# Optimization experiments

Measured on AMD Instinct MI355X. Metric: run time of the kernel, lower is better.

## Reference

```python
import jax, jax.numpy as jnp
import numpy as np

C, K, N = 128, 27, 4096   # channels, kernel offsets (3^3), parent points
M = 8 * N                  # child points (FCG: up to 8 children per parent)


def sp_conv(f, nbr, W):
    # sparse submanifold conv: gather K neighbors then per-offset GEMM
    # f: [P, C], nbr: [P, K], W: [K, C, C] -> [P, C]
    return jnp.einsum('pkc,kcd->pd', f[nbr], W)


def resnet(f, nbr, Wa, Wb):
    h = jax.nn.relu(sp_conv(f, nbr, Wa))
    return jax.nn.relu(sp_conv(h, nbr, Wb) + f)


def setup_inputs():
    key = jax.random.key(0)
    ks = jax.random.split(key, 30)
    conv = lambda k: jax.random.normal(k, (K, C, C), dtype=jnp.float32) * 0.02
    return {
        'x_O': jax.random.randint(ks[0], (N,), 0, 256, dtype=jnp.int32),
        'gt_O': jax.random.randint(ks[1], (M, 1), 0, 256, dtype=jnp.int32),
        'nbr_par': jax.random.randint(ks[2], (N, K), 0, N, dtype=jnp.int32),
        'nbr_child': jax.random.randint(ks[3], (M, K), 0, M, dtype=jnp.int32),
        'child_oct': jnp.tile(jnp.arange(8, dtype=jnp.int32), N),
        'prior_emb': jax.random.normal(ks[4], (256, C), dtype=jnp.float32),
        'pW0': conv(ks[5]), 'pW1a': conv(ks[6]), 'pW1b': conv(ks[7]),
        'pW2a': conv(ks[8]), 'pW2b': conv(ks[9]),
        'oct_emb': jax.random.normal(ks[10], (8, C), dtype=jnp.float32) * 0.1,
        'tW0': conv(ks[11]), 'tW1a': conv(ks[12]), 'tW1b': conv(ks[13]),
        'tW2a': conv(ks[14]), 'tW2b': conv(ks[15]),
        's1_emb': jax.random.normal(ks[16], (16, C), dtype=jnp.float32) * 0.1,
        'h0W1': jax.random.normal(ks[17], (C, C), dtype=jnp.float32) * 0.09,
        'h0b1': jnp.zeros((C,), dtype=jnp.float32),
        'h0W2': jax.random.normal(ks[18], (C, 16), dtype=jnp.float32) * 0.09,
        'h0b2': jnp.zeros((16,), dtype=jnp.float32),
        'h1W1': jax.random.normal(ks[19], (C, C), dtype=jnp.float32) * 0.09,
        'h1b1': jnp.zeros((C,), dtype=jnp.float32),
        'h1W2': jax.random.normal(ks[20], (C, 16), dtype=jnp.float32) * 0.09,
        'h1b2': jnp.zeros((16,), dtype=jnp.float32),
    }


def reference(x_O, gt_O, nbr_par, nbr_child, child_oct,
              prior_emb, pW0, pW1a, pW1b, pW2a, pW2b,
              oct_emb, tW0, tW1a, tW1b, tW2a, tW2b, s1_emb,
              h0W1, h0b1, h0W2, h0b2, h1W1, h1b1, h1W2, h1b2):
    # prior branch: occupancy byte embedding + sparse ResNet stack
    f = prior_emb[x_O]                                   # [N, C]
    f = jax.nn.relu(sp_conv(f, nbr_par, pW0))
    f = resnet(f, nbr_par, pW1a, pW1b)
    f = resnet(f, nbr_par, pW2a, pW2b)
    # FCG: broadcast parent feature to its 8 children; TargetEmbedding adds octant embedding
    g = jnp.repeat(f, 8, axis=0) + oct_emb[child_oct]    # [M, C]
    g = jax.nn.relu(sp_conv(g, nbr_child, tW0))
    g = resnet(g, nbr_child, tW1a, tW1b)
    g = resnet(g, nbr_child, tW2a, tW2b)
    # two-stage 4-bit occupancy prediction + gather-based entropy
    gt_s0 = jnp.remainder(gt_O, 16)                      # [M, 1]
    gt_s1 = gt_O // 16
    p0 = jax.nn.softmax(jax.nn.relu(g @ h0W1 + h0b1) @ h0W2 + h0b2, axis=-1)
    g1 = g + s1_emb[gt_s0[:, 0]]
    p1 = jax.nn.softmax(jax.nn.relu(g1 @ h1W1 + h1b1) @ h1W2 + h1b2, axis=-1)
    b0 = jnp.take_along_axis(p0, gt_s0, axis=1)
    b1 = jnp.take_along_axis(p1, gt_s1, axis=1)
    bits = (jnp.sum(jnp.clip(-jnp.log2(b0 + 1e-10), 0.0, 50.0))
            + jnp.sum(jnp.clip(-jnp.log2(b1 + 1e-10), 0.0, 50.0)))
    return bits / jnp.float32(N)
```

## Files before the change

kernel.cpp:

```cpp
#include <hip/hip_runtime.h>

typedef unsigned int u32;
typedef unsigned short u16;
typedef unsigned char u8;
typedef short bf16x8 __attribute__((ext_vector_type(8)));
typedef float f32x4 __attribute__((ext_vector_type(4)));
typedef unsigned short u16x4 __attribute__((ext_vector_type(4)));
typedef long lx2 __attribute__((ext_vector_type(2)));

#define KOFF 27

__device__ __forceinline__ float bf2f(u16 u) {
    u32 x = ((u32)u) << 16;
    return __builtin_bit_cast(float, x);
}
__device__ __forceinline__ u16 f2bf(float f) {
    u32 u = __builtin_bit_cast(u32, f);
    u32 r = (u + 0x7FFFu + ((u >> 16) & 1u)) >> 16;
    return (u16)r;
}
__device__ __forceinline__ u8 f2fp8(float f) {
    u32 u = __builtin_bit_cast(u32, f);
    u32 sign = (u >> 24) & 0x80u;
    float a = fabsf(f);
    if (a >= 448.f) return (u8)(sign | 0x7Eu);
    if (a < 0.015625f) {
        int q = (int)rintf(a * 512.f);
        return (u8)(sign | (u32)q);
    }
    u32 m = u & 0x7FFFFFFFu;
    m += 0x7FFFFu + ((m >> 20) & 1u);
    u32 e8 = (m >> 23) - 120u;
    if (e8 >= 16u) return (u8)(sign | 0x7Eu);
    return (u8)(sign | (e8 << 3) | ((m >> 20) & 7u));
}
__device__ __forceinline__ float fp82f(u8 v) {
    u32 s = ((u32)(v & 0x80)) << 24;
    u32 em = v & 0x7Fu;
    float mag;
    if (em < 8)
        mag = (float)em * 0.001953125f;
    else
        mag = __builtin_bit_cast(float,
                                 (((em >> 3) + 120u) << 23) | ((em & 7u) << 20));
    return __builtin_bit_cast(float, __builtin_bit_cast(u32, mag) | s);
}
__device__ __forceinline__ void async16(void* lds, const void* g) {
    __builtin_amdgcn_global_load_lds(
        (const __attribute__((address_space(1))) u32*)g,
        (__attribute__((address_space(3))) u32*)lds, 16, 0, 0);
}

struct PrepArgs {
    const float* ws[12];
    u16* wd[12];
    u8* wd3[5];
    const float* h0W2;
    const float* h1W2;
    u16* wt2h;
    const float* s1emb;
    const float* h1W1f;
    float* E1;
};
__global__ __launch_bounds__(256) void prep_mega(PrepArgs a) {
    __shared__ float t[128][65];
    const int bid = blockIdx.x;
    if (bid < 270) {
        const int w = bid / 54, r = bid % 54;
        const int k = r >> 1, cg = r & 1;
        const float* s = a.ws[w] + k * 16384 + cg * 64;
        for (int i = threadIdx.x; i < 8192; i += 256) {
            int c = i >> 6, dl = i & 63;
            t[c][dl] = s[c * 128 + dl];
        }
        __syncthreads();
        u16* ob = a.wd[w] + k * 16384;
        for (int sl = threadIdx.x; sl < 1024; sl += 256) {
            int lane = sl & 63, kk2 = (sl >> 6) & 1, n = (sl >> 7) & 3,
                kslc = (sl >> 9) & 1;
            int S = (((kslc * 2 + cg) * 4 + n) * 2 + kk2) * 64 + lane;
            int dl = n * 16 + (lane & 15);
            int c0 = kslc * 64 + kk2 * 32 + (lane >> 4) * 8;
            u16x4 v0, v1;
#pragma unroll
            for (int j = 0; j < 4; ++j) v0[j] = f2bf(t[c0 + j][dl]);
#pragma unroll
            for (int j = 0; j < 4; ++j) v1[j] = f2bf(t[c0 + 4 + j][dl]);
            *(u16x4*)(ob + S * 8) = v0;
            *(u16x4*)(ob + S * 8 + 4) = v1;
        }
    } else if (bid < 540) {
        const int idx = bid - 270;
        const int w5 = idx / 54, r = idx % 54;
        const int k = r >> 1, cg = r & 1;
        const float* s = a.ws[5 + w5] + k * 16384 + cg * 64;
        for (int i = threadIdx.x; i < 8192; i += 256) {
            int c = i >> 6, dl = i & 63;
            t[c][dl] = s[c * 128 + dl];
        }
        __syncthreads();
        u8* ob = a.wd3[w5] + k * 16384;
        for (int sl = threadIdx.x; sl < 8192; sl += 256) {
            int j = sl & 7, lane = (sl >> 3) & 63, kk2 = (sl >> 9) & 1,
                n = (sl >> 10) & 3, kslc = (sl >> 12) & 1;
            int c = kslc * 64 + kk2 * 32 + (lane >> 4) * 8 + j;
            int dl = n * 16 + (lane & 15);
            int byte = (kslc * 2 + cg) * 4096 + n * 1024 + lane * 16 + kk2 * 8 + j;
            ob[byte] = f2fp8(t[c][dl]);
        }
    } else if (bid < 544) {
        int r = bid - 540;
        int w = 10 + (r >> 1), half = r & 1;
        const float* s = a.ws[w] + half * 64;
        for (int i = threadIdx.x; i < 8192; i += 256) {
            int c = i >> 6, dl = i & 63;
            t[c][dl] = s[c * 128 + dl];
        }
        __syncthreads();
        u16* db = a.wd[w];
        for (int i = threadIdx.x; i < 8192; i += 256) {
            int dl = i >> 7, c = i & 127;
            int d = half * 64 + dl;
            db[d * 128 + (c ^ ((d & 7) << 3))] = f2bf(t[c][dl]);
        }
    } else if (bid < 546) {
        int h = bid - 544;
        const float* src = h ? a.h1W2 : a.h0W2;
        u16* dst = a.wt2h + h * 2048;
        for (int i = threadIdx.x; i < 2048; i += 256) {
            int j = i >> 7, d = i & 127;
            dst[j * 128 + (d ^ ((j & 7) << 3))] = f2bf(src[d * 16 + j]);
        }
    } else {
        int b = bid - 546;
        int r = b * 2 + (threadIdx.x >> 7);
        int c = threadIdx.x & 127;
        float acc = 0.f;
        for (int kx = 0; kx < 128; ++kx)
            acc = fmaf(a.s1emb[r * 128 + kx], a.h1W1f[kx * 128 + c], acc);
        a.E1[r * 128 + c] = acc;
    }
}

__global__ __launch_bounds__(256) void embed_k(const int* __restrict__ xO,
                                               const float* __restrict__ emb,
                                               u16* __restrict__ out) {
    int idx = blockIdx.x * 256 + threadIdx.x;
    int c = idx & 127, n = idx >> 7;
    out[idx] = f2bf(emb[xO[n] * 128 + c]);
}

__global__ __launch_bounds__(256) void expand8(const u16* __restrict__ f,
                                               const int* __restrict__ oct,
                                               const float* __restrict__ oemb,
                                               u8* __restrict__ g) {
    int idx = blockIdx.x * 256 + threadIdx.x;
    int c = idx & 127, m = idx >> 7;
    g[idx] = f2fp8(bf2f(f[(m >> 3) * 128 + c]) + oemb[oct[m] * 128 + c]);
}

#define LOADB(dst, vb, imm)                                      \
    asm volatile("global_load_dwordx4 %0, %1, %2 offset:" #imm   \
                 : "=&v"(dst)                                    \
                 : "v"(vb), "s"(wk)                              \
                 : "memory")

template <bool PARTIAL>
__global__ __launch_bounds__(256, 2) void conv7(
    const u16* __restrict__ fin, const int* __restrict__ nbr,
    const u16* __restrict__ wt, const u16* __restrict__ res,
    u16* __restrict__ fout, float* __restrict__ pout, int npts) {
    constexpr int BM = 64;
    __shared__ __align__(16) u16 Asb[2][4][4096];
    __shared__ int nbrS[BM * KOFF];
    const int tid = threadIdx.x;
    const int wid = tid >> 6;
    const int lane = tid & 63;
    const int p0 = blockIdx.x * BM;
    const int g = PARTIAL ? blockIdx.y : 0;
    const int k0 = PARTIAL ? (g * KOFF) >> 3 : 0;
    const int k1 = PARTIAL ? ((g + 1) * KOFF) >> 3 : KOFF;

    for (int i = tid; i < BM * KOFF; i += 256)
        nbrS[i] = nbr[(p0 + i / KOFF) * KOFF + (i % KOFF)];
    __syncthreads();

    f32x4 acc[2][4];
#pragma unroll
    for (int m = 0; m < 2; ++m)
#pragma unroll
        for (int n = 0; n < 4; ++n) acc[m][n] = f32x4{0.f, 0.f, 0.f, 0.f};

    const int rg0 = (wid >> 1) * 32;
    const int cg = wid & 1;
    const int lrow = lane & 15;
    const int lkb = (lane >> 4) * 16;
    const int b0a = cg * 8192 + lane * 16;
    const int b0b = b0a + 4096;
    const int b1a = b0a + 16384;
    const int b1b = b1a + 4096;

    auto stageA = [&](int k, int buf) {
        char* db = (char*)&Asb[buf][wid][0];
#pragma unroll
        for (int i = 0; i < 8; ++i) {
            int rl = i * 4 + (lane >> 4);
            int cbs = ((lane & 15) * 16) ^ ((rl & 7) << 4);
            int rgl = nbrS[(rg0 + rl) * KOFF + k];
            async16(db + i * 1024, (const char*)fin + (size_t)rgl * 256 + cbs);
        }
    };
    auto loadB = [&](int k, bf16x8 (&B)[16]) {
        const u16* wk = wt + k * 16384;
        LOADB(B[0], b0a, 0);
        LOADB(B[1], b0a, 1024);
        LOADB(B[2], b1a, 0);
        LOADB(B[3], b1a, 1024);
        LOADB(B[4], b0a, 2048);
        LOADB(B[5], b0a, 3072);
        LOADB(B[6], b1a, 2048);
        LOADB(B[7], b1a, 3072);
        LOADB(B[8], b0b, 0);
        LOADB(B[9], b0b, 1024);
        LOADB(B[10], b1b, 0);
        LOADB(B[11], b1b, 1024);
        LOADB(B[12], b0b, 2048);
        LOADB(B[13], b0b, 3072);
        LOADB(B[14], b1b, 2048);
        LOADB(B[15], b1b, 3072);
    };

    bf16x8 Ba[16], Bb[16];
    stageA(k0, 0);
    loadB(k0, Ba);

    auto body = [&](bf16x8 (&Bc)[16], bf16x8 (&Bn)[16], int k) {
        const int ab = (k - k0) & 1;
        if (k + 1 < k1) {
            stageA(k + 1, ab ^ 1);
            loadB(k + 1, Bn);
            asm volatile("s_waitcnt vmcnt(24)" ::: "memory");
        } else {
            asm volatile("s_waitcnt vmcnt(0)" ::: "memory");
        }
        __builtin_amdgcn_sched_barrier(0);
        const char* AsW = (const char*)&Asb[ab][wid][0];
        __builtin_amdgcn_s_setprio(1);
#pragma unroll
        for (int kk = 0; kk < 4; ++kk) {
            bf16x8 av[2];
#pragma unroll
            for (int m = 0; m < 2; ++m) {
                int row = m * 16 + lrow;
                int cb = (kk * 64 + lkb) ^ ((row & 7) << 4);
                av[m] = *(const bf16x8*)(AsW + row * 256 + cb);
            }
#pragma unroll
            for (int m = 0; m < 2; ++m)
#pragma unroll
                for (int n = 0; n < 4; ++n)
                    acc[m][n] = __builtin_amdgcn_mfma_f32_16x16x32_bf16(
                        av[m], Bc[n * 4 + kk], acc[m][n], 0, 0, 0);
        }
        __builtin_amdgcn_s_setprio(0);
    };

    int k = k0;
    while (true) {
        body(Ba, Bb, k);
        if (++k >= k1) break;
        body(Bb, Ba, k);
        if (++k >= k1) break;
    }

    if constexpr (PARTIAL) {
        float* pg = pout + (size_t)g * npts * 128;
#pragma unroll
        for (int m = 0; m < 2; ++m) {
            int prow = p0 + rg0 + m * 16 + (lane >> 4) * 4;
#pragma unroll
            for (int n = 0; n < 4; ++n) {
                int dcol = cg * 64 + n * 16 + lrow;
#pragma unroll
                for (int q = 0; q < 4; ++q)
                    pg[(prow + q) * 128 + dcol] = acc[m][n][q];
            }
        }
    } else {
#pragma unroll
        for (int m = 0; m < 2; ++m) {
            int prow = p0 + rg0 + m * 16 + (lane >> 4) * 4;
#pragma unroll
            for (int n = 0; n < 4; ++n) {
                int dcol = cg * 64 + n * 16 + lrow;
#pragma unroll
                for (int q = 0; q < 4; ++q) {
                    float v = acc[m][n][q];
                    int p = prow + q;
                    if (res) v += bf2f(res[p * 128 + dcol]);
                    v = v > 0.f ? v : 0.f;
                    fout[p * 128 + dcol] = f2bf(v);
                }
            }
        }
    }
}

template <bool LASTBF16>
__global__ __launch_bounds__(256, 4) void conv9(
    const u8* __restrict__ fin, const int* __restrict__ nbr,
    const u8* __restrict__ wt, const u8* __restrict__ res,
    void* __restrict__ fout_) {
    constexpr int BM = 32;
    __shared__ __align__(16) u8 Asb[2][BM * 128];
    __shared__ float red[4096];
    __shared__ int nbrS[BM * KOFF];
    const int tid = threadIdx.x;
    const int wid = tid >> 6;
    const int lane = tid & 63;
    const int p0 = blockIdx.x * BM;

    for (int i = tid; i < BM * KOFF; i += 256)
        nbrS[i] = nbr[(p0 + i / KOFF) * KOFF + (i % KOFF)];
    __syncthreads();

    f32x4 acc[2][4];
#pragma unroll
    for (int m = 0; m < 2; ++m)
#pragma unroll
        for (int n = 0; n < 4; ++n) acc[m][n] = f32x4{0.f, 0.f, 0.f, 0.f};

    const int kslc = wid >> 1;
    const int CB = (wid & 1) * 64;
    const int lrow = lane & 15;
    const int vb = (kslc * 2 + (wid & 1)) * 4096 + lane * 16;

    auto stageA = [&](int k, int buf) {
        int rl = wid * 8 + (lane >> 3);
        int boff = (lane & 7) * 16;
        int rg = nbrS[rl * KOFF + k];
        async16((char*)&Asb[buf][0] + wid * 1024,
                (const char*)fin + (size_t)rg * 128 + (boff ^ ((rl & 7) << 4)));
    };
    auto loadB = [&](int k, lx2 (&B)[4]) {
        const u8* wk = wt + k * 16384;
        LOADB(B[0], vb, 0);
        LOADB(B[1], vb, 1024);
        LOADB(B[2], vb, 2048);
        LOADB(B[3], vb, 3072);
    };

    lx2 Ba4[4], Bb4[4];
    stageA(0, 0);
    loadB(0, Ba4);

    auto body = [&](lx2 (&Bc)[4], lx2 (&Bn)[4], int k) {
        const int ab = k & 1;
        __builtin_amdgcn_s_barrier();
        if (k + 1 < KOFF) {
            loadB(k + 1, Bn);
            stageA(k + 1, ab ^ 1);
            asm volatile("s_waitcnt vmcnt(5)" ::: "memory");
        } else {
            asm volatile("s_waitcnt vmcnt(0)" ::: "memory");
        }
        __builtin_amdgcn_s_barrier();
        __builtin_amdgcn_sched_barrier(0);
        __builtin_amdgcn_s_setprio(1);
#pragma unroll
        for (int kk2 = 0; kk2 < 2; ++kk2) {
            long av[2];
#pragma unroll
            for (int m = 0; m < 2; ++m) {
                int row = m * 16 + lrow;
                int off = (kslc * 64 + kk2 * 32 + (lane >> 4) * 8) ^
                          ((row & 7) << 4);
                av[m] = *(const long*)((const char*)&Asb[ab][0] + row * 128 + off);
            }
#pragma unroll
            for (int m = 0; m < 2; ++m)
#pragma unroll
                for (int n = 0; n < 4; ++n)
                    acc[m][n] = __builtin_amdgcn_mfma_f32_16x16x32_fp8_fp8(
                        av[m], Bc[n][kk2], acc[m][n], 0, 0, 0);
        }
        __builtin_amdgcn_s_setprio(0);
    };

    int k = 0;
    while (true) {
        body(Ba4, Bb4, k);
        if (++k >= KOFF) break;
        body(Bb4, Ba4, k);
        if (++k >= KOFF) break;
    }

    __syncthreads();
    if (kslc == 1) {
        const int base = (wid - 2) * 2048;
#pragma unroll
        for (int m = 0; m < 2; ++m)
#pragma unroll
            for (int n = 0; n < 4; ++n)
#pragma unroll
                for (int q = 0; q < 4; ++q)
                    red[base + (((m * 4 + n) * 4 + q) * 64) + lane] =
                        acc[m][n][q];
    }
    __syncthreads();
    if (kslc == 0) {
        const int base = wid * 2048;
#pragma unroll
        for (int m = 0; m < 2; ++m)
#pragma unroll
            for (int n = 0; n < 4; ++n)
#pragma unroll
                for (int q = 0; q < 4; ++q)
                    acc[m][n][q] +=
                        red[base + (((m * 4 + n) * 4 + q) * 64) + lane];
#pragma unroll
        for (int m = 0; m < 2; ++m) {
            int prow = p0 + m * 16 + (lane >> 4) * 4;
#pragma unroll
            for (int n = 0; n < 4; ++n) {
                int dcol = CB + n * 16 + lrow;
#pragma unroll
                for (int q = 0; q < 4; ++q) {
                    float v = acc[m][n][q];
                    int p = prow + q;
                    if (res) v += fp82f(res[p * 128 + dcol]);
                    v = v > 0.f ? v : 0.f;
                    if constexpr (LASTBF16)
                        ((u16*)fout_)[p * 128 + dcol] = f2bf(v);
                    else
                        ((u8*)fout_)[p * 128 + dcol] = f2fp8(v);
                }
            }
        }
    }
}

__global__ __launch_bounds__(256) void combine_k(const float* __restrict__ P,
                                                 const u16* __restrict__ res,
                                                 u16* __restrict__ fout,
                                                 int nelem) {
    int base = (blockIdx.x * 256 + threadIdx.x) * 4;
    f32x4 s = *(const f32x4*)(P + base);
#pragma unroll
    for (int gg = 1; gg < 8; ++gg)
        s += *(const f32x4*)(P + (size_t)gg * nelem + base);
    u16x4 o;
    if (res) {
        u16x4 rv = *(const u16x4*)(res + base);
#pragma unroll
        for (int j = 0; j < 4; ++j) s[j] += bf2f(rv[j]);
    }
#pragma unroll
    for (int j = 0; j < 4; ++j) {
        float v = s[j] > 0.f ? s[j] : 0.f;
        o[j] = f2bf(v);
    }
    *(u16x4*)(fout + base) = o;
}

__global__ __launch_bounds__(512, 1) void fused_heads(
    const u16* __restrict__ G, const int* __restrict__ gtO,
    const u16* __restrict__ wt2, const u16* __restrict__ wt2h,
    const float* __restrict__ b1a, const float* __restrict__ b1b,
    const float* __restrict__ E1, const float* __restrict__ b2a,
    const float* __restrict__ b2b, float* __restrict__ partial) {
    __shared__ __align__(16) u16 AB[49152];
    __shared__ __align__(16) u16 W2ts[4096];
    __shared__ float E1s[2048];
    __shared__ float b2s[32];
    __shared__ int gts[256];
    __shared__ float bitsS[256];
    u16* Asb = AB;
    u16* Bsb = AB + 16384;
    char* Hb = (char*)AB;
    const int tid = threadIdx.x, wid = tid >> 6, lane = tid & 63;
    const int lrow = lane & 15, lkb = (lane >> 4) * 16;
    const int p0 = blockIdx.x * 128;

#pragma unroll
    for (int i = 0; i < 4; ++i) {
        int o = i * 8192 + tid * 16;
        int r = o >> 8;
        int cbs = (o & 255) ^ ((r & 7) << 4);
        async16((char*)Asb + i * 8192 + wid * 1024,
                (const char*)G + (size_t)(p0 + r) * 256 + cbs);
    }
#pragma unroll
    for (int i = 0; i < 8; ++i)
        async16((char*)Bsb + i * 8192 + wid * 1024,
                (const char*)wt2 + i * 8192 + tid * 16);
    async16((char*)W2ts + wid * 1024, (const char*)wt2h + tid * 16);
    for (int i = tid; i < 2048; i += 512) E1s[i] = E1[i];
    if (tid < 16) b2s[tid] = b2a[tid];
    else if (tid < 32) b2s[tid] = b2b[tid - 16];
    if (tid < 128) {
        int g = gtO[p0 + tid];
        gts[tid] = g & 15;
        gts[128 + tid] = g >> 4;
    }
    __syncthreads();

    const int RB = (wid >> 1) * 32, CB = (wid & 1) * 128;
    f32x4 acc[2][8];
#pragma unroll
    for (int m = 0; m < 2; ++m)
#pragma unroll
        for (int n = 0; n < 8; ++n) acc[m][n] = f32x4{0.f, 0.f, 0.f, 0.f};
    __builtin_amdgcn_s_setprio(1);
#pragma unroll
    for (int kk = 0; kk < 4; ++kk) {
        bf16x8 av[2], bv[8];
#pragma unroll
        for (int m = 0; m < 2; ++m) {
            int row = RB + m * 16 + lrow;
            int cb = (kk * 64 + lkb) ^ ((row & 7) << 4);
            av[m] = *(const bf16x8*)((const char*)Asb + row * 256 + cb);
        }
#pragma unroll
        for (int n = 0; n < 8; ++n) {
            int drow = CB + n * 16 + lrow;
            int cb = (kk * 64 + lkb) ^ ((drow & 7) << 4);
            bv[n] = *(const bf16x8*)((const char*)Bsb + drow * 256 + cb);
        }
#pragma unroll
        for (int m = 0; m < 2; ++m)
#pragma unroll
            for (int n = 0; n < 8; ++n)
                acc[m][n] = __builtin_amdgcn_mfma_f32_16x16x32_bf16(
                    av[m], bv[n], acc[m][n], 0, 0, 0);
    }
    __builtin_amdgcn_s_setprio(0);
    __syncthreads();

    const float* b1p = CB ? b1b : b1a;
    float b1v[8];
#pragma unroll
    for (int n = 0; n < 8; ++n) b1v[n] = b1p[n * 16 + lrow];
#pragma unroll
    for (int m = 0; m < 2; ++m) {
#pragma unroll
        for (int q = 0; q < 4; ++q) {
            int p = RB + m * 16 + (lane >> 4) * 4 + q;
#pragma unroll
            for (int n = 0; n < 8; ++n) {
                float v = acc[m][n][q] + b1v[n];
                if (CB) v += E1s[gts[p] * 128 + n * 16 + lrow];
                v = v > 0.f ? v : 0.f;
                int colb = (CB + n * 16 + lrow) * 2;
                *(u16*)(Hb + p * 512 + (colb ^ ((p & 7) << 4))) = f2bf(v);
            }
        }
    }
    __syncthreads();

    const int RB2 = wid * 16;
    f32x4 acc2[2];
    acc2[0] = f32x4{0.f, 0.f, 0.f, 0.f};
    acc2[1] = f32x4{0.f, 0.f, 0.f, 0.f};
#pragma unroll
    for (int kk = 0; kk < 4; ++kk) {
        int row = RB2 + lrow;
        int cb = (kk * 64 + lkb) ^ ((row & 7) << 4);
        int cbw = (kk * 64 + lkb) ^ ((lrow & 7) << 4);
#pragma unroll
        for (int h = 0; h < 2; ++h) {
            bf16x8 a2 = *(const bf16x8*)(Hb + row * 512 + h * 256 + cb);
            bf16x8 b2v = *(const bf16x8*)((const char*)W2ts + h * 4096 +
                                          lrow * 256 + cbw);
            acc2[h] = __builtin_amdgcn_mfma_f32_16x16x32_bf16(a2, b2v, acc2[h],
                                                              0, 0, 0);
        }
    }
    const int jj = lrow;
#pragma unroll
    for (int h = 0; h < 2; ++h) {
#pragma unroll
        for (int q = 0; q < 4; ++q) {
            int pt = RB2 + (lane >> 4) * 4 + q;
            float v = acc2[h][q] + b2s[h * 16 + jj];
            float mx = v;
#pragma unroll
            for (int o = 1; o < 16; o <<= 1) mx = fmaxf(mx, __shfl_xor(mx, o, 16));
            float e = expf(v - mx);
            float s = e;
#pragma unroll
            for (int o = 1; o < 16; o <<= 1) s += __shfl_xor(s, o, 16);
            float bits = -log2f(e / s + 1e-10f);
            bits = fminf(fmaxf(bits, 0.f), 50.f);
            if (jj == gts[h * 128 + pt]) bitsS[h * 128 + pt] = bits;
        }
    }
    __syncthreads();
    if (tid < 64) {
        float s = bitsS[tid] + bitsS[tid + 64] + bitsS[tid + 128] + bitsS[tid + 192];
#pragma unroll
        for (int o = 32; o > 0; o >>= 1) s += __shfl_down(s, o, 64);
        if (tid == 0) partial[blockIdx.x] = s;
    }
}

__global__ __launch_bounds__(256) void finalize_k(const float* __restrict__ partial,
                                                  float* __restrict__ out, int n) {
    float s = 0.f;
    for (int i = threadIdx.x; i < n; i += 256) s += partial[i];
#pragma unroll
    for (int o = 32; o > 0; o >>= 1) s += __shfl_down(s, o, 64);
    __shared__ float wsum[4];
    if ((threadIdx.x & 63) == 0) wsum[threadIdx.x >> 6] = s;
    __syncthreads();
    if (threadIdx.x == 0)
        out[0] = (wsum[0] + wsum[1] + wsum[2] + wsum[3]) * (1.0f / 4096.0f);
}

extern "C" void kernel_launch(void* const* d_in, const int* in_sizes, int n_in,
                              void* d_out, int out_size, void* d_ws,
                              size_t ws_size, hipStream_t stream) {
    const int N = 4096, M = 32768;
    const int* x_O = (const int*)d_in[0];
    const int* gt_O = (const int*)d_in[1];
    const int* nbr_par = (const int*)d_in[2];
    const int* nbr_ch = (const int*)d_in[3];
    const int* child_oct = (const int*)d_in[4];
    const float* prior_emb = (const float*)d_in[5];
    const float* convW[10] = {
        (const float*)d_in[6],  (const float*)d_in[7],  (const float*)d_in[8],
        (const float*)d_in[9],  (const float*)d_in[10], (const float*)d_in[12],
        (const float*)d_in[13], (const float*)d_in[14], (const float*)d_in[15],
        (const float*)d_in[16]};
    const float* oct_emb = (const float*)d_in[11];
    const float* s1_emb = (const float*)d_in[17];
    const float* h0W1 = (const float*)d_in[18];
    const float* h0b1 = (const float*)d_in[19];
    const float* h0W2 = (const float*)d_in[20];
    const float* h0b2 = (const float*)d_in[21];
    const float* h1W1 = (const float*)d_in[22];
    const float* h1b1 = (const float*)d_in[23];
    const float* h1W2 = (const float*)d_in[24];
    const float* h1b2 = (const float*)d_in[25];

    char* ws = (char*)d_ws;
    size_t off = 0;
    auto alloc = [&](size_t b) {
        void* p = ws + off;
        off += (b + 255) & ~(size_t)255;
        return p;
    };
    PrepArgs pa;
    for (int i = 0; i < 10; ++i) pa.ws[i] = convW[i];
    for (int i = 0; i < 5; ++i) pa.wd[i] = (u16*)alloc(27 * 128 * 128 * 2);
    for (int i = 5; i < 10; ++i) pa.wd[i] = nullptr;
    for (int i = 0; i < 5; ++i) pa.wd3[i] = (u8*)alloc(27 * 128 * 128);
    u16* Wt2 = (u16*)alloc(256 * 128 * 2);
    pa.ws[10] = h0W1;
    pa.ws[11] = h1W1;
    pa.wd[10] = Wt2;
    pa.wd[11] = Wt2 + 128 * 128;
    u16* wt2h = (u16*)alloc(2 * 16 * 128 * 2);
    float* E1 = (float*)alloc(16 * 128 * 4);
    pa.h0W2 = h0W2;
    pa.h1W2 = h1W2;
    pa.wt2h = wt2h;
    pa.s1emb = s1_emb;
    pa.h1W1f = h1W1;
    pa.E1 = E1;

    u16* fA = (u16*)alloc((size_t)N * 256);
    u16* fB = (u16*)alloc((size_t)N * 256);
    u16* fC = (u16*)alloc((size_t)N * 256);
    u8* g8A = (u8*)alloc((size_t)M * 128);
    u8* g8B = (u8*)alloc((size_t)M * 128);
    u8* g8C = (u8*)alloc((size_t)M * 128);
    u16* gBF = (u16*)alloc((size_t)M * 256);
    float* partial = (float*)alloc(256 * 4);
    float* pconv = (float*)g8A;

    prep_mega<<<554, 256, 0, stream>>>(pa);
    embed_k<<<N * 128 / 256, 256, 0, stream>>>(x_O, prior_emb, fA);

    const int PE = N * 128;
    conv7<true><<<dim3(64, 8), 256, 0, stream>>>(fA, nbr_par, pa.wd[0], nullptr, nullptr, pconv, N);
    combine_k<<<PE / 1024, 256, 0, stream>>>(pconv, nullptr, fB, PE);
    conv7<true><<<dim3(64, 8), 256, 0, stream>>>(fB, nbr_par, pa.wd[1], nullptr, nullptr, pconv, N);
    combine_k<<<PE / 1024, 256, 0, stream>>>(pconv, nullptr, fC, PE);
    conv7<true><<<dim3(64, 8), 256, 0, stream>>>(fC, nbr_par, pa.wd[2], nullptr, nullptr, pconv, N);
    combine_k<<<PE / 1024, 256, 0, stream>>>(pconv, fB, fA, PE);
    conv7<true><<<dim3(64, 8), 256, 0, stream>>>(fA, nbr_par, pa.wd[3], nullptr, nullptr, pconv, N);
    combine_k<<<PE / 1024, 256, 0, stream>>>(pconv, nullptr, fC, PE);
    conv7<true><<<dim3(64, 8), 256, 0, stream>>>(fC, nbr_par, pa.wd[4], nullptr, nullptr, pconv, N);
    combine_k<<<PE / 1024, 256, 0, stream>>>(pconv, fA, fB, PE);

    expand8<<<M * 128 / 256, 256, 0, stream>>>(fB, child_oct, oct_emb, g8A);

    conv9<false><<<1024, 256, 0, stream>>>(g8A, nbr_ch, pa.wd3[0], nullptr, g8B);
    conv9<false><<<1024, 256, 0, stream>>>(g8B, nbr_ch, pa.wd3[1], nullptr, g8C);
    conv9<false><<<1024, 256, 0, stream>>>(g8C, nbr_ch, pa.wd3[2], g8B, g8A);
    conv9<false><<<1024, 256, 0, stream>>>(g8A, nbr_ch, pa.wd3[3], nullptr, g8C);
    conv9<true><<<1024, 256, 0, stream>>>(g8C, nbr_ch, pa.wd3[4], g8A, gBF);

    fused_heads<<<M / 128, 512, 0, stream>>>(gBF, gt_O, Wt2, wt2h, h0b1, h1b1,
                                             E1, h0b2, h1b2, partial);
    finalize_k<<<1, 256, 0, stream>>>(partial, (float*)d_out, 256);

    (void)in_sizes; (void)n_in; (void)out_size; (void)ws_size;
}
```

Before: 301.5 us.

## Shrink child conv tile to 16 rows with two-wave K-split blocks

Replaces the 32-row, 4-wave child-conv kernel with a 16-row, 2-wave variant. Each wave covers all 128 output columns for its half of the input channels and loads twice as many weight fragments. The grid doubles to 2048 blocks, which should improve occupancy and load balance across CUs and shrink LDS use per block. The cost is that each weight byte is reused across only 16 rows instead of 32, so weight traffic from L2 doubles, and each wave holds more B registers.

```diff
diff --git a/kernel.cpp b/kernel.cpp
--- a/kernel.cpp
+++ b/kernel.cpp
@@ -307,33 +307,31 @@
 }
 
 template <bool LASTBF16>
-__global__ __launch_bounds__(256, 4) void conv9(
+__global__ __launch_bounds__(128, 4) void conv12(
     const u8* __restrict__ fin, const int* __restrict__ nbr,
     const u8* __restrict__ wt, const u8* __restrict__ res,
     void* __restrict__ fout_) {
-    constexpr int BM = 32;
+    constexpr int BM = 16;
     __shared__ __align__(16) u8 Asb[2][BM * 128];
-    __shared__ float red[4096];
+    __shared__ float red[2048];
     __shared__ int nbrS[BM * KOFF];
     const int tid = threadIdx.x;
     const int wid = tid >> 6;
     const int lane = tid & 63;
     const int p0 = blockIdx.x * BM;
 
-    for (int i = tid; i < BM * KOFF; i += 256)
+    for (int i = tid; i < BM * KOFF; i += 128)
         nbrS[i] = nbr[(p0 + i / KOFF) * KOFF + (i % KOFF)];
     __syncthreads();
 
-    f32x4 acc[2][4];
-#pragma unroll
-    for (int m = 0; m < 2; ++m)
-#pragma unroll
-        for (int n = 0; n < 4; ++n) acc[m][n] = f32x4{0.f, 0.f, 0.f, 0.f};
-
-    const int kslc = wid >> 1;
-    const int CB = (wid & 1) * 64;
+    f32x4 acc[8];
+#pragma unroll
+    for (int n = 0; n < 8; ++n) acc[n] = f32x4{0.f, 0.f, 0.f, 0.f};
+
+    const int kslc = wid;
     const int lrow = lane & 15;
-    const int vb = (kslc * 2 + (wid & 1)) * 4096 + lane * 16;
+    const int vb0 = kslc * 8192 + lane * 16;
+    const int vb1 = vb0 + 4096;
 
     auto stageA = [&](int k, int buf) {
         int rl = wid * 8 + (lane >> 3);
@@ -342,99 +340,85 @@
         async16((char*)&Asb[buf][0] + wid * 1024,
                 (const char*)fin + (size_t)rg * 128 + (boff ^ ((rl & 7) << 4)));
     };
-    auto loadB = [&](int k, lx2 (&B)[4]) {
+    auto loadB = [&](int k, lx2 (&B)[8]) {
         const u8* wk = wt + k * 16384;
-        LOADB(B[0], vb, 0);
-        LOADB(B[1], vb, 1024);
-        LOADB(B[2], vb, 2048);
-        LOADB(B[3], vb, 3072);
+        LOADB(B[0], vb0, 0);
+        LOADB(B[1], vb0, 1024);
+        LOADB(B[2], vb0, 2048);
+        LOADB(B[3], vb0, 3072);
+        LOADB(B[4], vb1, 0);
+        LOADB(B[5], vb1, 1024);
+        LOADB(B[6], vb1, 2048);
+        LOADB(B[7], vb1, 3072);
     };
 
-    lx2 Ba4[4], Bb4[4];
+    lx2 Ba8[8], Bb8[8];
+    loadB(0, Ba8);
     stageA(0, 0);
-    loadB(0, Ba4);
-
-    auto body = [&](lx2 (&Bc)[4], lx2 (&Bn)[4], int k) {
+
+    auto body = [&](lx2 (&Bc)[8], lx2 (&Bn)[8], int k) {
         const int ab = k & 1;
         __builtin_amdgcn_s_barrier();
         if (k + 1 < KOFF) {
             loadB(k + 1, Bn);
             stageA(k + 1, ab ^ 1);
-            asm volatile("s_waitcnt vmcnt(5)" ::: "memory");
+            asm volatile("s_waitcnt vmcnt(9)" ::: "memory");
         } else {
             asm volatile("s_waitcnt vmcnt(0)" ::: "memory");
         }
         __builtin_amdgcn_s_barrier();
         __builtin_amdgcn_sched_barrier(0);
         __builtin_amdgcn_s_setprio(1);
+        const u8* As = &Asb[ab][0];
 #pragma unroll
         for (int kk2 = 0; kk2 < 2; ++kk2) {
-            long av[2];
-#pragma unroll
-            for (int m = 0; m < 2; ++m) {
-                int row = m * 16 + lrow;
-                int off = (kslc * 64 + kk2 * 32 + (lane >> 4) * 8) ^
-                          ((row & 7) << 4);
-                av[m] = *(const long*)((const char*)&Asb[ab][0] + row * 128 + off);
-            }
-#pragma unroll
-            for (int m = 0; m < 2; ++m)
-#pragma unroll
-                for (int n = 0; n < 4; ++n)
-                    acc[m][n] = __builtin_amdgcn_mfma_f32_16x16x32_fp8_fp8(
-                        av[m], Bc[n][kk2], acc[m][n], 0, 0, 0);
+            int off = (kslc * 64 + kk2 * 32 + (lane >> 4) * 8) ^
+                      ((lrow & 7) << 4);
+            long av = *(const long*)((const char*)As + lrow * 128 + off);
+#pragma unroll
+            for (int n = 0; n < 8; ++n)
+                acc[n] = __builtin_amdgcn_mfma_f32_16x16x32_fp8_fp8(
+                    av, Bc[n][kk2], acc[n], 0, 0, 0);
         }
         __builtin_amdgcn_s_setprio(0);
     };
 
     int k = 0;
     while (true) {
-        body(Ba4, Bb4, k);
+        body(Ba8, Bb8, k);
         if (++k >= KOFF) break;
-        body(Bb4, Ba4, k);
+        body(Bb8, Ba8, k);
         if (++k >= KOFF) break;
     }
 
     __syncthreads();
     if (kslc == 1) {
-        const int base = (wid - 2) * 2048;
-#pragma unroll
-        for (int m = 0; m < 2; ++m)
-#pragma unroll
-            for (int n = 0; n < 4; ++n)
-#pragma unroll
-                for (int q = 0; q < 4; ++q)
-                    red[base + (((m * 4 + n) * 4 + q) * 64) + lane] =
-                        acc[m][n][q];
+#pragma unroll
+        for (int n = 0; n < 8; ++n)
+#pragma unroll
+            for (int q = 0; q < 4; ++q)
+                red[(n * 4 + q) * 64 + lane] = acc[n][q];
     }
     __syncthreads();
     if (kslc == 0) {
-        const int base = wid * 2048;
-#pragma unroll
-        for (int m = 0; m < 2; ++m)
-#pragma unroll
-            for (int n = 0; n < 4; ++n)
-#pragma unroll
-                for (int q = 0; q < 4; ++q)
-                    acc[m][n][q] +=
-                        red[base + (((m * 4 + n) * 4 + q) * 64) + lane];
-#pragma unroll
-        for (int m = 0; m < 2; ++m) {
-            int prow = p0 + m * 16 + (lane >> 4) * 4;
-#pragma unroll
-            for (int n = 0; n < 4; ++n) {
-                int dcol = CB + n * 16 + lrow;
-#pragma unroll
-                for (int q = 0; q < 4; ++q) {
-                    float v = acc[m][n][q];
-                    int p = prow + q;
-                    if (res) v += fp82f(res[p * 128 + dcol]);
-                    v = v > 0.f ? v : 0.f;
-                    if constexpr (LASTBF16)
-                        ((u16*)fout_)[p * 128 + dcol] = f2bf(v);
-                    else
-                        ((u8*)fout_)[p * 128 + dcol] = f2fp8(v);
-                }
+#pragma unroll
+        for (int n = 0; n < 8; ++n)
+#pragma unroll
+            for (int q = 0; q < 4; ++q)
+                acc[n][q] += red[(n * 4 + q) * 64 + lane];
+#pragma unroll
+        for (int n = 0; n < 8; ++n) {
+            int dcol = n * 16 + lrow;
+#pragma unroll
+            for (int q = 0; q < 4; ++q) {
+                int p = p0 + (lane >> 4) * 4 + q;
+                float v = acc[n][q];
+                if (res) v += fp82f(res[p * 128 + dcol]);
+                v = v > 0.f ? v : 0.f;
+                if constexpr (LASTBF16)
+                    ((u16*)fout_)[p * 128 + dcol] = f2bf(v);
+                else
+                    ((u8*)fout_)[p * 128 + dcol] = f2fp8(v);
             }
         }
     }
@@ -696,11 +680,11 @@
 
     expand8<<<M * 128 / 256, 256, 0, stream>>>(fB, child_oct, oct_emb, g8A);
 
-    conv9<false><<<1024, 256, 0, stream>>>(g8A, nbr_ch, pa.wd3[0], nullptr, g8B);
-    conv9<false><<<1024, 256, 0, stream>>>(g8B, nbr_ch, pa.wd3[1], nullptr, g8C);
-    conv9<false><<<1024, 256, 0, stream>>>(g8C, nbr_ch, pa.wd3[2], g8B, g8A);
-    conv9<false><<<1024, 256, 0, stream>>>(g8A, nbr_ch, pa.wd3[3], nullptr, g8C);
-    conv9<true><<<1024, 256, 0, stream>>>(g8C, nbr_ch, pa.wd3[4], g8A, gBF);
+    conv12<false><<<2048, 128, 0, stream>>>(g8A, nbr_ch, pa.wd3[0], nullptr, g8B);
+    conv12<false><<<2048, 128, 0, stream>>>(g8B, nbr_ch, pa.wd3[1], nullptr, g8C);
+    conv12<false><<<2048, 128, 0, stream>>>(g8C, nbr_ch, pa.wd3[2], g8B, g8A);
+    conv12<false><<<2048, 128, 0, stream>>>(g8A, nbr_ch, pa.wd3[3], nullptr, g8C);
+    conv12<true><<<2048, 128, 0, stream>>>(g8C, nbr_ch, pa.wd3[4], g8A, gBF);
 
     fused_heads<<<M / 128, 512, 0, stream>>>(gBF, gt_O, Wt2, wt2h, h0b1, h1b1,
                                              E1, h0b2, h1b2, partial);
```

After: 735.0 us. +143.8%, slower.
